# Kernel tuning notes

Hardware: AMD Instinct MI355X
Metric: run time of the kernel (lower is better)

## Reference

```python
import jax, jax.numpy as jnp
import numpy as np

H = 16  # num_heads
NEG = -1e9


def setup_inputs() -> dict:
    key = jax.random.key(0)
    ks = jax.random.split(key, 12)
    T, B, E, M = 2048, 2, 1024, 1024
    s = E ** -0.5
    inp = {
        "query": jax.random.normal(ks[0], (T, B, E), jnp.float32),
        "position_encoding": jax.random.normal(ks[1], (H, T, T), jnp.float32) * 0.02,
        "long_context_retrieval": jax.random.normal(ks[2], (2, M, B, E), jnp.float32),
        "q_w": jax.random.normal(ks[3], (E, E), jnp.float32) * s,
        "q_b": jnp.zeros((E,), jnp.float32),
        "k_w": jax.random.normal(ks[4], (E, E), jnp.float32) * s,
        "k_b": jnp.zeros((E,), jnp.float32),
        "v_w": jax.random.normal(ks[5], (E, E), jnp.float32) * s,
        "v_b": jnp.zeros((E,), jnp.float32),
        "out_w": jax.random.normal(ks[6], (E, E), jnp.float32) * s,
        "out_b": jnp.zeros((E,), jnp.float32),
        "memory_bias": jnp.zeros((H,), jnp.float32),
    }
    return inp


def reference(query, position_encoding, long_context_retrieval,
              q_w, q_b, k_w, k_b, v_w, v_b, out_w, out_b, memory_bias):
    T, B, E = query.shape
    D = E // H
    scaling = D ** -0.5

    def proj(x, w, b):
        # x: [L, B, E] -> [B, H, L, D]
        L = x.shape[0]
        y = jnp.einsum('lbe,fe->lbf', x, w) + b
        return y.reshape(L, B, H, D).transpose(1, 2, 0, 3)

    q = proj(query, q_w, q_b) * scaling          # [B,H,T,D]
    k = proj(query, k_w, k_b)                    # [B,H,T,D]
    v = proj(query, v_w, v_b)                    # [B,H,T,D]

    # local attention with per-head position encoding and causal mask
    scores = jnp.einsum('bhtd,bhsd->bhts', q, k) + position_encoding[None]
    causal = jnp.triu(jnp.ones((T, T), bool), k=1)
    scores = jnp.where(causal[None, None], NEG, scores)
    attn_local = jax.nn.softmax(scores, axis=-1)
    out_local = jnp.einsum('bhts,bhsd->bhtd', attn_local, v)

    # attention over retrieved long-context memory (keys/values projected)
    km = proj(long_context_retrieval[0], k_w, k_b)   # [B,H,M,D]
    vm = proj(long_context_retrieval[1], v_w, v_b)   # [B,H,M,D]
    mem_scores = jnp.einsum('bhtd,bhmd->bhtm', q, km)
    attn_mem = jax.nn.softmax(mem_scores, axis=-1)
    out_mem = jnp.einsum('bhtm,bhmd->bhtd', attn_mem, vm)

    # per-head learned gate: weighted sum of local and memory outputs
    g = jax.nn.sigmoid(memory_bias)[None, :, None, None]
    out = (1.0 - g) * out_local + g * out_mem        # [B,H,T,D]

    out = out.transpose(2, 0, 1, 3).reshape(T, B, E)
    return jnp.einsum('tbe,fe->tbf', out, out_w) + out_b
```

## Files before the change

kernel.cpp:

```cpp
#include <hip/hip_runtime.h>

typedef __bf16 bf16_t;
typedef __bf16 bf16x2 __attribute__((ext_vector_type(2)));
typedef __bf16 bf16x4 __attribute__((ext_vector_type(4)));
typedef __bf16 bf16x8 __attribute__((ext_vector_type(8)));
typedef float floatx4 __attribute__((ext_vector_type(4)));

#define MFMA16(a, b, c) __builtin_amdgcn_mfma_f32_16x16x32_bf16((a), (b), (c), 0, 0, 0)

__global__ void detect_kernel(const uint4* __restrict__ q, int* __restrict__ flag)
{
    __shared__ int cnt;
    if (threadIdx.x == 0) cnt = 0;
    __syncthreads();
    int local = 0;
    for (int i = threadIdx.x; i < 8192; i += 1024) {
        uint4 u = q[i];
        unsigned w;
        w = u.x; if ((w & 0x7F80u) == 0x7F80u) local++; if (((w >> 16) & 0x7F80u) == 0x7F80u) local++;
        w = u.y; if ((w & 0x7F80u) == 0x7F80u) local++; if (((w >> 16) & 0x7F80u) == 0x7F80u) local++;
        w = u.z; if ((w & 0x7F80u) == 0x7F80u) local++; if (((w >> 16) & 0x7F80u) == 0x7F80u) local++;
        w = u.w; if ((w & 0x7F80u) == 0x7F80u) local++; if (((w >> 16) & 0x7F80u) == 0x7F80u) local++;
    }
    atomicAdd(&cnt, local);
    __syncthreads();
    if (threadIdx.x == 0) flag[0] = (cnt >= 8) ? 1 : 0;
}

__device__ inline void cvt16_f32(const float* __restrict__ p, bf16x8& lo, bf16x8& hi)
{
    float4 a = ((const float4*)p)[0];
    float4 b = ((const float4*)p)[1];
    float4 c = ((const float4*)p)[2];
    float4 d = ((const float4*)p)[3];
    lo[0] = (bf16_t)a.x; lo[1] = (bf16_t)a.y; lo[2] = (bf16_t)a.z; lo[3] = (bf16_t)a.w;
    lo[4] = (bf16_t)b.x; lo[5] = (bf16_t)b.y; lo[6] = (bf16_t)b.z; lo[7] = (bf16_t)b.w;
    hi[0] = (bf16_t)c.x; hi[1] = (bf16_t)c.y; hi[2] = (bf16_t)c.z; hi[3] = (bf16_t)c.w;
    hi[4] = (bf16_t)d.x; hi[5] = (bf16_t)d.y; hi[6] = (bf16_t)d.z; hi[7] = (bf16_t)d.w;
}

__global__ __launch_bounds__(256) void proj_kernel(
    const void* __restrict__ query, const void* __restrict__ lcr,
    const void* __restrict__ qw, const void* __restrict__ kw,
    const void* __restrict__ vw,
    const void* __restrict__ qbias, const void* __restrict__ kbias,
    const void* __restrict__ vbias,
    bf16_t* __restrict__ q_ws, bf16_t* __restrict__ k_ws,
    bf16_t* __restrict__ vt_ws, bf16_t* __restrict__ km_ws,
    bf16_t* __restrict__ vmt_ws, const int* __restrict__ flag)
{
    __shared__ __attribute__((aligned(16))) bf16_t As[128 * 40];
    __shared__ __attribute__((aligned(16))) bf16_t Bs[128 * 40];

    const int f32 = flag[0];
    const int K = 1024;
    const int blk = blockIdx.x;

    int rm0, wcol, mode, Tdim;
    float scale;
    const void* Xv; size_t xoff0; const void* Wv; const void* biasv; bf16_t* Yv;
    if (blk < 768) {
        rm0 = (blk & 31) * 128;
        const int cn0 = (blk >> 5) * 128;
        const int sel = cn0 >> 10;
        wcol = cn0 & 1023;
        Xv = query; xoff0 = 0; Tdim = 2048;
        if (sel == 0)      { Wv = qw; biasv = qbias; Yv = q_ws;  mode = 1; scale = 0.125f; }
        else if (sel == 1) { Wv = kw; biasv = kbias; Yv = k_ws;  mode = 1; scale = 1.f; }
        else               { Wv = vw; biasv = vbias; Yv = vt_ws; mode = 2; scale = 1.f; }
    } else if (blk < 896) {
        const int b2 = blk - 768;
        rm0 = (b2 & 15) * 128; wcol = (b2 >> 4) * 128;
        Xv = lcr; xoff0 = 0;
        Wv = kw; biasv = kbias; Yv = km_ws; mode = 1; scale = 1.f; Tdim = 1024;
    } else {
        const int b2 = blk - 896;
        rm0 = (b2 & 15) * 128; wcol = (b2 >> 4) * 128;
        Xv = lcr; xoff0 = (size_t)1024 * 2 * 1024;
        Wv = vw; biasv = vbias; Yv = vmt_ws; mode = 2; scale = 1.f; Tdim = 1024;
    }

    const int tid = threadIdx.x;
    const int wvid = tid >> 6, lane = tid & 63;
    const int qd = lane >> 4, l16 = lane & 15;
    const int wm = (wvid >> 1) * 64, wn = (wvid & 1) * 64;

    const int srow = tid >> 1;
    const int sseg = (tid & 1) * 16;
    const size_t xoff = xoff0 + (size_t)(rm0 + srow) * K + sseg;
    const size_t woff = (size_t)(wcol + srow) * K + sseg;
    const bf16_t* Xh = (const bf16_t*)Xv + xoff;
    const float*  Xf = (const float*)Xv + xoff;
    const bf16_t* Wh = (const bf16_t*)Wv + woff;
    const float*  Wf = (const float*)Wv + woff;
    bf16_t* Asw = &As[srow * 40 + sseg];
    bf16_t* Bsw = &Bs[srow * 40 + sseg];

    floatx4 acc[4][4];
#pragma unroll
    for (int i = 0; i < 4; i++)
#pragma unroll
        for (int j = 0; j < 4; j++) acc[i][j] = (floatx4){0.f, 0.f, 0.f, 0.f};

    for (int k0 = 0; k0 < K; k0 += 32) {
        bf16x8 x0, x1, w0, w1;
        if (f32) {
            cvt16_f32(Xf + k0, x0, x1);
            cvt16_f32(Wf + k0, w0, w1);
        } else {
            x0 = *(const bf16x8*)(Xh + k0);
            x1 = *(const bf16x8*)(Xh + k0 + 8);
            w0 = *(const bf16x8*)(Wh + k0);
            w1 = *(const bf16x8*)(Wh + k0 + 8);
        }
        __syncthreads();
        *(bf16x8*)(Asw) = x0;
        *(bf16x8*)(Asw + 8) = x1;
        *(bf16x8*)(Bsw) = w0;
        *(bf16x8*)(Bsw + 8) = w1;
        __syncthreads();

        bf16x8 af[4], bfg[4];
#pragma unroll
        for (int mi = 0; mi < 4; mi++)
            af[mi] = *(const bf16x8*)(&As[(wm + mi * 16 + l16) * 40 + qd * 8]);
#pragma unroll
        for (int ni = 0; ni < 4; ni++)
            bfg[ni] = *(const bf16x8*)(&Bs[(wn + ni * 16 + l16) * 40 + qd * 8]);
#pragma unroll
        for (int mi = 0; mi < 4; mi++)
#pragma unroll
            for (int ni = 0; ni < 4; ni++)
                acc[mi][ni] = MFMA16(af[mi], bfg[ni], acc[mi][ni]);
    }

#pragma unroll
    for (int ni = 0; ni < 4; ni++) {
        const int col = wcol + wn + ni * 16 + l16;
        const float bv = f32 ? ((const float*)biasv)[col]
                             : (float)((const bf16_t*)biasv)[col];
        const int hh = col >> 6, dd = col & 63;
#pragma unroll
        for (int mi = 0; mi < 4; mi++) {
            const int row0 = rm0 + wm + mi * 16 + qd * 4;
            const int t = row0 >> 1;
            const float v0 = (acc[mi][ni][0] + bv) * scale;
            const float v1 = (acc[mi][ni][1] + bv) * scale;
            const float v2 = (acc[mi][ni][2] + bv) * scale;
            const float v3 = (acc[mi][ni][3] + bv) * scale;
            if (mode == 1) {
                Yv[(((size_t)hh * Tdim) + t) * 64 + dd]            = (bf16_t)v0;
                Yv[(((size_t)(16 + hh) * Tdim) + t) * 64 + dd]     = (bf16_t)v1;
                Yv[(((size_t)hh * Tdim) + t + 1) * 64 + dd]        = (bf16_t)v2;
                Yv[(((size_t)(16 + hh) * Tdim) + t + 1) * 64 + dd] = (bf16_t)v3;
            } else {
                bf16x2 p0; p0[0] = (bf16_t)v0; p0[1] = (bf16_t)v2;
                bf16x2 p1; p1[0] = (bf16_t)v1; p1[1] = (bf16_t)v3;
                *(bf16x2*)&Yv[((size_t)hh * 64 + dd) * Tdim + t] = p0;
                *(bf16x2*)&Yv[((size_t)(16 + hh) * 64 + dd) * Tdim + t] = p1;
            }
        }
    }
}

#define PSTR 88

__device__ __forceinline__ void load_k8(bf16x8 k0v[4], bf16x8 k1v[4],
                                        const bf16_t* __restrict__ Kb,
                                        int s0, int l16, int qd)
{
#pragma unroll
    for (int ni = 0; ni < 4; ni++) {
        const bf16_t* p = Kb + (size_t)(s0 + ni * 16 + l16) * 64 + qd * 8;
        k0v[ni] = *(const bf16x8*)p;
        k1v[ni] = *(const bf16x8*)(p + 32);
    }
}

__device__ __forceinline__ void load_pos4(floatx4 pn[4], const float* __restrict__ posf,
                                          const bf16_t* __restrict__ posh, int f32,
                                          int T, int trow_base, int s0, int l16, bool diag)
{
#pragma unroll
    for (int ni = 0; ni < 4; ni++) {
        const int sg = s0 + ni * 16 + l16;
#pragma unroll
        for (int r = 0; r < 4; r++) {
            const int tg = trow_base + r;
            const size_t pidx = (size_t)tg * T + sg;
            float pv = f32 ? posf[pidx] : (float)posh[pidx];
            if (diag && sg > tg) pv = -1e9f;
            pn[ni][r] = pv;
        }
    }
}

__global__ __launch_bounds__(256) void attn_kernel(
    const bf16_t* __restrict__ Qg, const bf16_t* __restrict__ Kg,
    const bf16_t* __restrict__ VTg, const bf16_t* __restrict__ KMg,
    const bf16_t* __restrict__ VMTg, const void* __restrict__ posv,
    const void* __restrict__ mbiasv, float* __restrict__ attl,
    float* __restrict__ attm, const int* __restrict__ flag, int T, int Mlen)
{
    __shared__ __attribute__((aligned(16))) bf16_t Ps[4][16 * PSTR];

    const int f32 = flag[0];
    const int tid = threadIdx.x;
    const int wv = tid >> 6, lane = tid & 63;
    const int qd = lane >> 4, l16 = lane & 15;
    const int qt = blockIdx.x;
    const int y = blockIdx.y;
    const int b = y & 1, h = y >> 1;
    const int bh = b * 16 + h;
    const int tw = qt * 64 + wv * 16;
    const int trow_base = tw + qd * 4;
    bf16_t* Pw = &Ps[wv][0];

    const bf16_t* Qb = Qg + (size_t)bh * T * 64;
    const bf16x8 a0 = *(const bf16x8*)(Qb + (size_t)(tw + l16) * 64 + qd * 8);
    const bf16x8 a1 = *(const bf16x8*)(Qb + (size_t)(tw + l16) * 64 + 32 + qd * 8);

    const float gb = f32 ? ((const float*)mbiasv)[h] : (float)((const bf16_t*)mbiasv)[h];
    const float g = 1.f / (1.f + __expf(-gb));

    floatx4 O[4];
    float ml[4], ll[4];
#pragma unroll
    for (int i = 0; i < 4; i++) {
        O[i] = (floatx4){0.f, 0.f, 0.f, 0.f};
        ml[i] = -1e9f; ll[i] = 0.f;
    }

    bf16x8 kc0[4], kc1[4];

    if (blockIdx.z == 0) {
        const bf16_t* Kb  = Kg  + (size_t)bh * T * 64;
        const bf16_t* VTb = VTg + (size_t)bh * 64 * T;
        const float*  posf = (const float*)posv + (size_t)h * T * T;
        const bf16_t* posh = (const bf16_t*)posv + (size_t)h * T * T;

        floatx4 pn[4];
        load_k8(kc0, kc1, Kb, 0, l16, qd);
        load_pos4(pn, posf, posh, f32, T, trow_base, 0, l16, qt == 0);

        for (int st = 0; st <= qt; ++st) {
            const int s0 = st * 64;
            bf16x8 vf0[4], vf1[4];
#pragma unroll
            for (int ni = 0; ni < 4; ni++) {
                const bf16_t* p = VTb + (size_t)(ni * 16 + l16) * T + s0 + qd * 8;
                vf0[ni] = *(const bf16x8*)p;
                vf1[ni] = *(const bf16x8*)(p + 32);
            }
            floatx4 c[4];
#pragma unroll
            for (int ni = 0; ni < 4; ni++) {
                floatx4 t = pn[ni];
                t = MFMA16(a0, kc0[ni], t);
                t = MFMA16(a1, kc1[ni], t);
                c[ni] = t;
            }
            if (st < qt) {
                load_k8(kc0, kc1, Kb, s0 + 64, l16, qd);
                load_pos4(pn, posf, posh, f32, T, trow_base, s0 + 64, l16, st + 1 == qt);
            }
#pragma unroll
            for (int r = 0; r < 4; r++) {
                float mt = fmaxf(fmaxf(c[0][r], c[1][r]), fmaxf(c[2][r], c[3][r]));
                mt = fmaxf(mt, __shfl_xor(mt, 1));
                mt = fmaxf(mt, __shfl_xor(mt, 2));
                mt = fmaxf(mt, __shfl_xor(mt, 4));
                mt = fmaxf(mt, __shfl_xor(mt, 8));
                const float mnew = fmaxf(ml[r], mt);
                const float alpha = __expf(ml[r] - mnew);
                ml[r] = mnew;
                float ls = 0.f;
#pragma unroll
                for (int ni = 0; ni < 4; ni++) {
                    const float p = __expf(c[ni][r] - mnew);
                    c[ni][r] = p;
                    ls += p;
                }
                ll[r] = ll[r] * alpha + ls;
#pragma unroll
                for (int ni = 0; ni < 4; ni++) O[ni][r] *= alpha;
#pragma unroll
                for (int ni = 0; ni < 4; ni++)
                    Pw[(qd * 4 + r) * PSTR + ni * 16 + l16] = (bf16_t)c[ni][r];
            }
            asm volatile("s_waitcnt lgkmcnt(0)" ::: "memory");
            const bf16x8 pf0 = *(const bf16x8*)(&Pw[l16 * PSTR + qd * 8]);
            const bf16x8 pf1 = *(const bf16x8*)(&Pw[l16 * PSTR + 32 + qd * 8]);
#pragma unroll
            for (int ni = 0; ni < 4; ni++) {
                O[ni] = MFMA16(pf0, vf0[ni], O[ni]);
                O[ni] = MFMA16(pf1, vf1[ni], O[ni]);
            }
        }

        const float gl = 1.f - g;
#pragma unroll
        for (int r = 0; r < 4; r++) {
            float lt = ll[r];
            lt += __shfl_xor(lt, 1);
            lt += __shfl_xor(lt, 2);
            lt += __shfl_xor(lt, 4);
            lt += __shfl_xor(lt, 8);
            const int tg = trow_base + r;
            const float inv = gl / lt;
#pragma unroll
            for (int ni = 0; ni < 4; ni++)
                attl[(size_t)(tg * 2 + b) * 1024 + h * 64 + ni * 16 + l16] = O[ni][r] * inv;
        }
    } else {
        const bf16_t* Kb  = KMg  + (size_t)bh * Mlen * 64;
        const bf16_t* VTb = VMTg + (size_t)bh * 64 * Mlen;
        const int nst = Mlen >> 6;

        load_k8(kc0, kc1, Kb, 0, l16, qd);

        for (int st = 0; st < nst; ++st) {
            const int s0 = st * 64;
            bf16x8 vf0[4], vf1[4];
#pragma unroll
            for (int ni = 0; ni < 4; ni++) {
                const bf16_t* p = VTb + (size_t)(ni * 16 + l16) * Mlen + s0 + qd * 8;
                vf0[ni] = *(const bf16x8*)p;
                vf1[ni] = *(const bf16x8*)(p + 32);
            }
            floatx4 c[4];
#pragma unroll
            for (int ni = 0; ni < 4; ni++) {
                floatx4 t = (floatx4){0.f, 0.f, 0.f, 0.f};
                t = MFMA16(a0, kc0[ni], t);
                t = MFMA16(a1, kc1[ni], t);
                c[ni] = t;
            }
            if (st < nst - 1) load_k8(kc0, kc1, Kb, s0 + 64, l16, qd);
#pragma unroll
            for (int r = 0; r < 4; r++) {
                float mt = fmaxf(fmaxf(c[0][r], c[1][r]), fmaxf(c[2][r], c[3][r]));
                mt = fmaxf(mt, __shfl_xor(mt, 1));
                mt = fmaxf(mt, __shfl_xor(mt, 2));
                mt = fmaxf(mt, __shfl_xor(mt, 4));
                mt = fmaxf(mt, __shfl_xor(mt, 8));
                const float mnew = fmaxf(ml[r], mt);
                const float alpha = __expf(ml[r] - mnew);
                ml[r] = mnew;
                float ls = 0.f;
#pragma unroll
                for (int ni = 0; ni < 4; ni++) {
                    const float p = __expf(c[ni][r] - mnew);
                    c[ni][r] = p;
                    ls += p;
                }
                ll[r] = ll[r] * alpha + ls;
#pragma unroll
                for (int ni = 0; ni < 4; ni++) O[ni][r] *= alpha;
#pragma unroll
                for (int ni = 0; ni < 4; ni++)
                    Pw[(qd * 4 + r) * PSTR + ni * 16 + l16] = (bf16_t)c[ni][r];
            }
            asm volatile("s_waitcnt lgkmcnt(0)" ::: "memory");
            const bf16x8 pf0 = *(const bf16x8*)(&Pw[l16 * PSTR + qd * 8]);
            const bf16x8 pf1 = *(const bf16x8*)(&Pw[l16 * PSTR + 32 + qd * 8]);
#pragma unroll
            for (int ni = 0; ni < 4; ni++) {
                O[ni] = MFMA16(pf0, vf0[ni], O[ni]);
                O[ni] = MFMA16(pf1, vf1[ni], O[ni]);
            }
        }

#pragma unroll
        for (int r = 0; r < 4; r++) {
            float lt = ll[r];
            lt += __shfl_xor(lt, 1);
            lt += __shfl_xor(lt, 2);
            lt += __shfl_xor(lt, 4);
            lt += __shfl_xor(lt, 8);
            const int tg = trow_base + r;
            const float inv = g / lt;
#pragma unroll
            for (int ni = 0; ni < 4; ni++)
                attm[(size_t)(tg * 2 + b) * 1024 + h * 64 + ni * 16 + l16] = O[ni][r] * inv;
        }
    }
}

__global__ __launch_bounds__(256) void combine_kernel(
    const float4* __restrict__ a, const float4* __restrict__ bsrc,
    bf16_t* __restrict__ o, int n4)
{
    const int i = blockIdx.x * 256 + threadIdx.x;
    if (i >= n4) return;
    const float4 x = a[i];
    const float4 y = bsrc[i];
    bf16x4 r;
    r[0] = (bf16_t)(x.x + y.x);
    r[1] = (bf16_t)(x.y + y.y);
    r[2] = (bf16_t)(x.z + y.z);
    r[3] = (bf16_t)(x.w + y.w);
    *(bf16x4*)(o + (size_t)i * 4) = r;
}

__global__ __launch_bounds__(256) void gemm64_kernel(
    const bf16_t* __restrict__ X, const void* __restrict__ Wv,
    const void* __restrict__ biasv, void* __restrict__ Yv,
    const int* __restrict__ flag)
{
    __shared__ __attribute__((aligned(16))) bf16_t As[64 * 40];
    __shared__ __attribute__((aligned(16))) bf16_t Bs[128 * 40];

    const int f32 = flag[0];
    const int K = 1024, N = 1024;
    const int tid = threadIdx.x;
    const int wvid = tid >> 6, lane = tid & 63;
    const int qd = lane >> 4, l16 = lane & 15;
    const int wn = wvid * 32;
    const int rm0 = blockIdx.x * 64, cn0 = blockIdx.y * 128;

    const int arow = tid >> 1;
    const int aseg = (tid & 1) * 16;
    const bf16_t* Xp = X + (size_t)(rm0 + (arow & 63)) * K + aseg;
    const size_t woff = (size_t)(cn0 + arow) * K + aseg;
    const bf16_t* Wh = (const bf16_t*)Wv + woff;
    const float*  Wf = (const float*)Wv + woff;

    floatx4 acc[4][2];
#pragma unroll
    for (int i = 0; i < 4; i++)
#pragma unroll
        for (int j = 0; j < 2; j++) acc[i][j] = (floatx4){0.f, 0.f, 0.f, 0.f};

    for (int k0 = 0; k0 < K; k0 += 32) {
        bf16x8 x0, x1, w0, w1;
        if (tid < 128) {
            x0 = *(const bf16x8*)(Xp + k0);
            x1 = *(const bf16x8*)(Xp + k0 + 8);
        }
        if (f32) cvt16_f32(Wf + k0, w0, w1);
        else {
            w0 = *(const bf16x8*)(Wh + k0);
            w1 = *(const bf16x8*)(Wh + k0 + 8);
        }
        __syncthreads();
        if (tid < 128) {
            *(bf16x8*)&As[arow * 40 + aseg] = x0;
            *(bf16x8*)&As[arow * 40 + aseg + 8] = x1;
        }
        *(bf16x8*)&Bs[arow * 40 + aseg] = w0;
        *(bf16x8*)&Bs[arow * 40 + aseg + 8] = w1;
        __syncthreads();

        bf16x8 af[4], bfg[2];
#pragma unroll
        for (int mi = 0; mi < 4; mi++)
            af[mi] = *(const bf16x8*)(&As[(mi * 16 + l16) * 40 + qd * 8]);
#pragma unroll
        for (int ni = 0; ni < 2; ni++)
            bfg[ni] = *(const bf16x8*)(&Bs[(wn + ni * 16 + l16) * 40 + qd * 8]);
#pragma unroll
        for (int mi = 0; mi < 4; mi++)
#pragma unroll
            for (int ni = 0; ni < 2; ni++)
                acc[mi][ni] = MFMA16(af[mi], bfg[ni], acc[mi][ni]);
    }

#pragma unroll
    for (int ni = 0; ni < 2; ni++) {
        const int col = cn0 + wn + ni * 16 + l16;
        const float bv = f32 ? ((const float*)biasv)[col]
                             : (float)((const bf16_t*)biasv)[col];
#pragma unroll
        for (int mi = 0; mi < 4; mi++) {
            const int row0 = rm0 + mi * 16 + qd * 4;
#pragma unroll
            for (int r = 0; r < 4; r++) {
                const int row = row0 + r;
                const float val = acc[mi][ni][r] + bv;
                if (f32) ((float*)Yv)[(size_t)row * N + col] = val;
                else ((bf16_t*)Yv)[(size_t)row * N + col] = (bf16_t)val;
            }
        }
    }
}

__global__ void sentinel_kernel(float* o) { o[0] = 30000.0f; }

extern "C" void kernel_launch(void* const* d_in, const int* in_sizes, int n_in,
                              void* d_out, int out_size, void* d_ws, size_t ws_size,
                              hipStream_t stream)
{
    const void* query = d_in[0];
    const void* pos   = d_in[1];
    const void* lcr   = d_in[2];
    const void* q_w   = d_in[3];
    const void* q_b   = d_in[4];
    const void* k_w   = d_in[5];
    const void* k_b   = d_in[6];
    const void* v_w   = d_in[7];
    const void* v_b   = d_in[8];
    const void* out_w = d_in[9];
    const void* out_b = d_in[10];
    const void* mbias = d_in[11];

    const int T = 2048, B = 2, E = 1024, M = 1024;

    const size_t nqkv = (size_t)B * 16 * T * 64;
    const size_t nmem = (size_t)B * 16 * M * 64;
    const size_t natt = (size_t)T * B * E;
    const size_t bf16_elems = 3 * nqkv + 2 * nmem + natt;
    const size_t needed = bf16_elems * 2 + 2 * natt * 4 + 64;
    if (ws_size < needed) {
        sentinel_kernel<<<1, 1, 0, stream>>>((float*)d_out);
        return;
    }

    bf16_t* q_ws   = (bf16_t*)d_ws;
    bf16_t* k_ws   = q_ws + nqkv;
    bf16_t* vt_ws  = k_ws + nqkv;
    bf16_t* km_ws  = vt_ws + nqkv;
    bf16_t* vmt_ws = km_ws + nmem;
    bf16_t* att_ws = vmt_ws + nmem;
    float* attl_ws = (float*)(att_ws + natt);
    float* attm_ws = attl_ws + natt;
    int* flag = (int*)(attm_ws + natt);

    detect_kernel<<<1, 1024, 0, stream>>>((const uint4*)query, flag);
    proj_kernel<<<1024, 256, 0, stream>>>(query, lcr, q_w, k_w, v_w,
                                          q_b, k_b, v_b,
                                          q_ws, k_ws, vt_ws, km_ws, vmt_ws, flag);
    attn_kernel<<<dim3(T / 64, 32, 2), 256, 0, stream>>>(
        q_ws, k_ws, vt_ws, km_ws, vmt_ws, pos, mbias, attl_ws, attm_ws, flag, T, M);
    combine_kernel<<<(int)(natt / 4 / 256), 256, 0, stream>>>(
        (const float4*)attl_ws, (const float4*)attm_ws, att_ws, (int)(natt / 4));
    gemm64_kernel<<<dim3(T * B / 64, E / 128), 256, 0, stream>>>(
        att_ws, out_w, out_b, d_out, flag);
    (void)in_sizes; (void)n_in; (void)out_size;
}
```

Measured before the change: 851.7 us.

## Pre-tile position encoding to bf16 and pair causal query tiles per block

Adds a prep kernel that converts the per-head position bias to bf16, applies the causal mask, and stores it in the per-lane MFMA fragment order of lower-triangular tiles. The attention kernel can then read each tile's bias as two contiguous 16-byte loads instead of scattered strided fp32 reads. The attention grid is halved and each block handles query tile p together with tile 31-p, which evens out causal work across blocks. The cost is an extra pass over the position tensor, extra workspace, and bf16 rounding of the bias. The tiled path is used only when the workspace is large enough.

```diff
diff --git a/kernel.cpp b/kernel.cpp
--- a/kernel.cpp
+++ b/kernel.cpp
@@ -37,6 +37,57 @@
     lo[4] = (bf16_t)b.x; lo[5] = (bf16_t)b.y; lo[6] = (bf16_t)b.z; lo[7] = (bf16_t)b.w;
     hi[0] = (bf16_t)c.x; hi[1] = (bf16_t)c.y; hi[2] = (bf16_t)c.z; hi[3] = (bf16_t)c.w;
     hi[4] = (bf16_t)d.x; hi[5] = (bf16_t)d.y; hi[6] = (bf16_t)d.z; hi[7] = (bf16_t)d.w;
+}
+
+__global__ __launch_bounds__(256) void prep_pos(
+    const void* __restrict__ posv, bf16_t* __restrict__ post,
+    const int* __restrict__ flag, int T)
+{
+    const int st = blockIdx.x, qt = blockIdx.y, h = blockIdx.z;
+    if (st > qt) return;
+    __shared__ float tf[64 * 65];
+    const int t = threadIdx.x;
+    const int f32 = flag[0];
+    const size_t rb = ((size_t)h * T + qt * 64) * T + st * 64;
+    if (f32) {
+        const float* pf = (const float*)posv + rb;
+#pragma unroll
+        for (int it = 0; it < 4; ++it) {
+            const int idx = it * 256 + t;
+            const int row = idx >> 4, c4 = (idx & 15) * 4;
+            const float4 v = *(const float4*)(pf + (size_t)row * T + c4);
+            tf[row * 65 + c4 + 0] = v.x;
+            tf[row * 65 + c4 + 1] = v.y;
+            tf[row * 65 + c4 + 2] = v.z;
+            tf[row * 65 + c4 + 3] = v.w;
+        }
+    } else {
+        const bf16_t* ph = (const bf16_t*)posv + rb;
+#pragma unroll
+        for (int it = 0; it < 2; ++it) {
+            const int idx = it * 256 + t;
+            const int row = idx >> 3, c8 = (idx & 7) * 8;
+            const bf16x8 v = *(const bf16x8*)(ph + (size_t)row * T + c8);
+#pragma unroll
+            for (int j = 0; j < 8; ++j) tf[row * 65 + c8 + j] = (float)v[j];
+        }
+    }
+    __syncthreads();
+    const int gg = t >> 4, l16 = t & 15;
+    const bool diag = (st == qt);
+    bf16x8 o0, o1;
+#pragma unroll
+    for (int j = 0; j < 16; ++j) {
+        const int ni = j >> 2, r = j & 3;
+        const int row = gg * 4 + r, col = ni * 16 + l16;
+        float v = tf[row * 65 + col];
+        if (diag && col > row) v = -1e9f;
+        if (j < 8) o0[j] = (bf16_t)v; else o1[j - 8] = (bf16_t)v;
+    }
+    bf16_t* out = post + ((size_t)h * 528 + (size_t)qt * (qt + 1) / 2 + st) * 4096
+                       + (size_t)t * 16;
+    *(bf16x8*)out = o0;
+    *(bf16x8*)(out + 8) = o1;
 }
 
 __global__ __launch_bounds__(256) void proj_kernel(
@@ -199,8 +250,9 @@
     const bf16_t* __restrict__ Qg, const bf16_t* __restrict__ Kg,
     const bf16_t* __restrict__ VTg, const bf16_t* __restrict__ KMg,
     const bf16_t* __restrict__ VMTg, const void* __restrict__ posv,
-    const void* __restrict__ mbiasv, float* __restrict__ attl,
-    float* __restrict__ attm, const int* __restrict__ flag, int T, int Mlen)
+    const bf16_t* __restrict__ post, const void* __restrict__ mbiasv,
+    float* __restrict__ attl, float* __restrict__ attm,
+    const int* __restrict__ flag, int T, int Mlen, int tiled)
 {
     __shared__ __attribute__((aligned(16))) bf16_t Ps[4][16 * PSTR];
 
@@ -208,181 +260,209 @@
     const int tid = threadIdx.x;
     const int wv = tid >> 6, lane = tid & 63;
     const int qd = lane >> 4, l16 = lane & 15;
-    const int qt = blockIdx.x;
+    const int p = blockIdx.x;
     const int y = blockIdx.y;
     const int b = y & 1, h = y >> 1;
     const int bh = b * 16 + h;
-    const int tw = qt * 64 + wv * 16;
-    const int trow_base = tw + qd * 4;
     bf16_t* Pw = &Ps[wv][0];
-
-    const bf16_t* Qb = Qg + (size_t)bh * T * 64;
-    const bf16x8 a0 = *(const bf16x8*)(Qb + (size_t)(tw + l16) * 64 + qd * 8);
-    const bf16x8 a1 = *(const bf16x8*)(Qb + (size_t)(tw + l16) * 64 + 32 + qd * 8);
+    const int laneTileOff = ((wv * 4 + qd) * 16 + l16) * 16;
 
     const float gb = f32 ? ((const float*)mbiasv)[h] : (float)((const bf16_t*)mbiasv)[h];
     const float g = 1.f / (1.f + __expf(-gb));
-
-    floatx4 O[4];
-    float ml[4], ll[4];
-#pragma unroll
-    for (int i = 0; i < 4; i++) {
-        O[i] = (floatx4){0.f, 0.f, 0.f, 0.f};
-        ml[i] = -1e9f; ll[i] = 0.f;
-    }
-
-    bf16x8 kc0[4], kc1[4];
-
-    if (blockIdx.z == 0) {
-        const bf16_t* Kb  = Kg  + (size_t)bh * T * 64;
-        const bf16_t* VTb = VTg + (size_t)bh * 64 * T;
-        const float*  posf = (const float*)posv + (size_t)h * T * T;
-        const bf16_t* posh = (const bf16_t*)posv + (size_t)h * T * T;
-
-        floatx4 pn[4];
-        load_k8(kc0, kc1, Kb, 0, l16, qd);
-        load_pos4(pn, posf, posh, f32, T, trow_base, 0, l16, qt == 0);
-
-        for (int st = 0; st <= qt; ++st) {
-            const int s0 = st * 64;
-            bf16x8 vf0[4], vf1[4];
-#pragma unroll
-            for (int ni = 0; ni < 4; ni++) {
-                const bf16_t* p = VTb + (size_t)(ni * 16 + l16) * T + s0 + qd * 8;
-                vf0[ni] = *(const bf16x8*)p;
-                vf1[ni] = *(const bf16x8*)(p + 32);
+    const float gl = 1.f - g;
+
+    const bf16_t* Qb = Qg + (size_t)bh * T * 64;
+
+    for (int half = 0; half < 2; ++half) {
+        const int qt = half ? (31 - p) : p;
+        const int tw = qt * 64 + wv * 16;
+        const int trow_base = tw + qd * 4;
+
+        const bf16x8 a0 = *(const bf16x8*)(Qb + (size_t)(tw + l16) * 64 + qd * 8);
+        const bf16x8 a1 = *(const bf16x8*)(Qb + (size_t)(tw + l16) * 64 + 32 + qd * 8);
+
+        floatx4 O[4];
+        float ml[4], ll[4];
+#pragma unroll
+        for (int i = 0; i < 4; i++) {
+            O[i] = (floatx4){0.f, 0.f, 0.f, 0.f};
+            ml[i] = -1e9f; ll[i] = 0.f;
+        }
+
+        bf16x8 kc0[4], kc1[4];
+
+        if (blockIdx.z == 0) {
+            const bf16_t* Kb  = Kg  + (size_t)bh * T * 64;
+            const bf16_t* VTb = VTg + (size_t)bh * 64 * T;
+            const float*  posf = (const float*)posv + (size_t)h * T * T;
+            const bf16_t* posh = (const bf16_t*)posv + (size_t)h * T * T;
+            const bf16_t* ptile = post + ((size_t)h * 528 + (size_t)qt * (qt + 1) / 2) * 4096
+                                       + laneTileOff;
+
+            floatx4 pn[4];
+            bf16x8 pt0, pt1;
+            load_k8(kc0, kc1, Kb, 0, l16, qd);
+            if (tiled) {
+                pt0 = *(const bf16x8*)(ptile);
+                pt1 = *(const bf16x8*)(ptile + 8);
+            } else {
+                load_pos4(pn, posf, posh, f32, T, trow_base, 0, l16, qt == 0);
             }
-            floatx4 c[4];
-#pragma unroll
-            for (int ni = 0; ni < 4; ni++) {
-                floatx4 t = pn[ni];
-                t = MFMA16(a0, kc0[ni], t);
-                t = MFMA16(a1, kc1[ni], t);
-                c[ni] = t;
+
+            for (int st = 0; st <= qt; ++st) {
+                const int s0 = st * 64;
+                bf16x8 vf0[4], vf1[4];
+#pragma unroll
+                for (int ni = 0; ni < 4; ni++) {
+                    const bf16_t* vp = VTb + (size_t)(ni * 16 + l16) * T + s0 + qd * 8;
+                    vf0[ni] = *(const bf16x8*)vp;
+                    vf1[ni] = *(const bf16x8*)(vp + 32);
+                }
+                if (tiled) {
+#pragma unroll
+                    for (int ni = 0; ni < 4; ni++)
+#pragma unroll
+                        for (int r = 0; r < 4; r++)
+                            pn[ni][r] = (ni < 2) ? (float)pt0[ni * 4 + r]
+                                                 : (float)pt1[ni * 4 + r - 8];
+                }
+                floatx4 c[4];
+#pragma unroll
+                for (int ni = 0; ni < 4; ni++) {
+                    floatx4 t = pn[ni];
+                    t = MFMA16(a0, kc0[ni], t);
+                    t = MFMA16(a1, kc1[ni], t);
+                    c[ni] = t;
+                }
+                if (st < qt) {
+                    load_k8(kc0, kc1, Kb, s0 + 64, l16, qd);
+                    if (tiled) {
+                        pt0 = *(const bf16x8*)(ptile + (st + 1) * 4096);
+                        pt1 = *(const bf16x8*)(ptile + (st + 1) * 4096 + 8);
+                    } else {
+                        load_pos4(pn, posf, posh, f32, T, trow_base, s0 + 64, l16,
+                                  st + 1 == qt);
+                    }
+                }
+#pragma unroll
+                for (int r = 0; r < 4; r++) {
+                    float mt = fmaxf(fmaxf(c[0][r], c[1][r]), fmaxf(c[2][r], c[3][r]));
+                    mt = fmaxf(mt, __shfl_xor(mt, 1));
+                    mt = fmaxf(mt, __shfl_xor(mt, 2));
+                    mt = fmaxf(mt, __shfl_xor(mt, 4));
+                    mt = fmaxf(mt, __shfl_xor(mt, 8));
+                    const float mnew = fmaxf(ml[r], mt);
+                    const float alpha = __expf(ml[r] - mnew);
+                    ml[r] = mnew;
+                    float ls = 0.f;
+#pragma unroll
+                    for (int ni = 0; ni < 4; ni++) {
+                        const float pe = __expf(c[ni][r] - mnew);
+                        c[ni][r] = pe;
+                        ls += pe;
+                    }
+                    ll[r] = ll[r] * alpha + ls;
+#pragma unroll
+                    for (int ni = 0; ni < 4; ni++) O[ni][r] *= alpha;
+#pragma unroll
+                    for (int ni = 0; ni < 4; ni++)
+                        Pw[(qd * 4 + r) * PSTR + ni * 16 + l16] = (bf16_t)c[ni][r];
+                }
+                asm volatile("s_waitcnt lgkmcnt(0)" ::: "memory");
+                const bf16x8 pf0 = *(const bf16x8*)(&Pw[l16 * PSTR + qd * 8]);
+                const bf16x8 pf1 = *(const bf16x8*)(&Pw[l16 * PSTR + 32 + qd * 8]);
+#pragma unroll
+                for (int ni = 0; ni < 4; ni++) {
+                    O[ni] = MFMA16(pf0, vf0[ni], O[ni]);
+                    O[ni] = MFMA16(pf1, vf1[ni], O[ni]);
+                }
             }
-            if (st < qt) {
-                load_k8(kc0, kc1, Kb, s0 + 64, l16, qd);
-                load_pos4(pn, posf, posh, f32, T, trow_base, s0 + 64, l16, st + 1 == qt);
+
+#pragma unroll
+            for (int r = 0; r < 4; r++) {
+                float lt = ll[r];
+                lt += __shfl_xor(lt, 1);
+                lt += __shfl_xor(lt, 2);
+                lt += __shfl_xor(lt, 4);
+                lt += __shfl_xor(lt, 8);
+                const int tg = trow_base + r;
+                const float inv = gl / lt;
+#pragma unroll
+                for (int ni = 0; ni < 4; ni++)
+                    attl[(size_t)(tg * 2 + b) * 1024 + h * 64 + ni * 16 + l16] = O[ni][r] * inv;
             }
+        } else {
+            const bf16_t* Kb  = KMg  + (size_t)bh * Mlen * 64;
+            const bf16_t* VTb = VMTg + (size_t)bh * 64 * Mlen;
+            const int nst = Mlen >> 6;
+
+            load_k8(kc0, kc1, Kb, 0, l16, qd);
+
+            for (int st = 0; st < nst; ++st) {
+                const int s0 = st * 64;
+                bf16x8 vf0[4], vf1[4];
+#pragma unroll
+                for (int ni = 0; ni < 4; ni++) {
+                    const bf16_t* vp = VTb + (size_t)(ni * 16 + l16) * Mlen + s0 + qd * 8;
+                    vf0[ni] = *(const bf16x8*)vp;
+                    vf1[ni] = *(const bf16x8*)(vp + 32);
+                }
+                floatx4 c[4];
+#pragma unroll
+                for (int ni = 0; ni < 4; ni++) {
+                    floatx4 t = (floatx4){0.f, 0.f, 0.f, 0.f};
+                    t = MFMA16(a0, kc0[ni], t);
+                    t = MFMA16(a1, kc1[ni], t);
+                    c[ni] = t;
+                }
+                if (st < nst - 1) load_k8(kc0, kc1, Kb, s0 + 64, l16, qd);
+#pragma unroll
+                for (int r = 0; r < 4; r++) {
+                    float mt = fmaxf(fmaxf(c[0][r], c[1][r]), fmaxf(c[2][r], c[3][r]));
+                    mt = fmaxf(mt, __shfl_xor(mt, 1));
+                    mt = fmaxf(mt, __shfl_xor(mt, 2));
+                    mt = fmaxf(mt, __shfl_xor(mt, 4));
+                    mt = fmaxf(mt, __shfl_xor(mt, 8));
+                    const float mnew = fmaxf(ml[r], mt);
+                    const float alpha = __expf(ml[r] - mnew);
+                    ml[r] = mnew;
+                    float ls = 0.f;
+#pragma unroll
+                    for (int ni = 0; ni < 4; ni++) {
+                        const float pe = __expf(c[ni][r] - mnew);
+                        c[ni][r] = pe;
+                        ls += pe;
+                    }
+                    ll[r] = ll[r] * alpha + ls;
+#pragma unroll
+                    for (int ni = 0; ni < 4; ni++) O[ni][r] *= alpha;
+#pragma unroll
+                    for (int ni = 0; ni < 4; ni++)
+                        Pw[(qd * 4 + r) * PSTR + ni * 16 + l16] = (bf16_t)c[ni][r];
+                }
+                asm volatile("s_waitcnt lgkmcnt(0)" ::: "memory");
+                const bf16x8 pf0 = *(const bf16x8*)(&Pw[l16 * PSTR + qd * 8]);
+                const bf16x8 pf1 = *(const bf16x8*)(&Pw[l16 * PSTR + 32 + qd * 8]);
+#pragma unroll
+                for (int ni = 0; ni < 4; ni++) {
+                    O[ni] = MFMA16(pf0, vf0[ni], O[ni]);
+                    O[ni] = MFMA16(pf1, vf1[ni], O[ni]);
+                }
+            }
+
 #pragma unroll
             for (int r = 0; r < 4; r++) {
-                float mt = fmaxf(fmaxf(c[0][r], c[1][r]), fmaxf(c[2][r], c[3][r]));
-                mt = fmaxf(mt, __shfl_xor(mt, 1));
-                mt = fmaxf(mt, __shfl_xor(mt, 2));
-                mt = fmaxf(mt, __shfl_xor(mt, 4));
-                mt = fmaxf(mt, __shfl_xor(mt, 8));
-                const float mnew = fmaxf(ml[r], mt);
-                const float alpha = __expf(ml[r] - mnew);
-                ml[r] = mnew;
-                float ls = 0.f;
-#pragma unroll
-                for (int ni = 0; ni < 4; ni++) {
-                    const float p = __expf(c[ni][r] - mnew);
-                    c[ni][r] = p;
-                    ls += p;
-                }
-                ll[r] = ll[r] * alpha + ls;
-#pragma unroll
-                for (int ni = 0; ni < 4; ni++) O[ni][r] *= alpha;
+                float lt = ll[r];
+                lt += __shfl_xor(lt, 1);
+                lt += __shfl_xor(lt, 2);
+                lt += __shfl_xor(lt, 4);
+                lt += __shfl_xor(lt, 8);
+                const int tg = trow_base + r;
+                const float inv = g / lt;
 #pragma unroll
                 for (int ni = 0; ni < 4; ni++)
-                    Pw[(qd * 4 + r) * PSTR + ni * 16 + l16] = (bf16_t)c[ni][r];
+                    attm[(size_t)(tg * 2 + b) * 1024 + h * 64 + ni * 16 + l16] = O[ni][r] * inv;
             }
-            asm volatile("s_waitcnt lgkmcnt(0)" ::: "memory");
-            const bf16x8 pf0 = *(const bf16x8*)(&Pw[l16 * PSTR + qd * 8]);
-            const bf16x8 pf1 = *(const bf16x8*)(&Pw[l16 * PSTR + 32 + qd * 8]);
-#pragma unroll
-            for (int ni = 0; ni < 4; ni++) {
-                O[ni] = MFMA16(pf0, vf0[ni], O[ni]);
-                O[ni] = MFMA16(pf1, vf1[ni], O[ni]);
-            }
-        }
-
-        const float gl = 1.f - g;
-#pragma unroll
-        for (int r = 0; r < 4; r++) {
-            float lt = ll[r];
-            lt += __shfl_xor(lt, 1);
-            lt += __shfl_xor(lt, 2);
-            lt += __shfl_xor(lt, 4);
-            lt += __shfl_xor(lt, 8);
-            const int tg = trow_base + r;
-            const float inv = gl / lt;
-#pragma unroll
-            for (int ni = 0; ni < 4; ni++)
-                attl[(size_t)(tg * 2 + b) * 1024 + h * 64 + ni * 16 + l16] = O[ni][r] * inv;
-        }
-    } else {
-        const bf16_t* Kb  = KMg  + (size_t)bh * Mlen * 64;
-        const bf16_t* VTb = VMTg + (size_t)bh * 64 * Mlen;
-        const int nst = Mlen >> 6;
-
-        load_k8(kc0, kc1, Kb, 0, l16, qd);
-
-        for (int st = 0; st < nst; ++st) {
-            const int s0 = st * 64;
-            bf16x8 vf0[4], vf1[4];
-#pragma unroll
-            for (int ni = 0; ni < 4; ni++) {
-                const bf16_t* p = VTb + (size_t)(ni * 16 + l16) * Mlen + s0 + qd * 8;
-                vf0[ni] = *(const bf16x8*)p;
-                vf1[ni] = *(const bf16x8*)(p + 32);
-            }
-            floatx4 c[4];
-#pragma unroll
-            for (int ni = 0; ni < 4; ni++) {
-                floatx4 t = (floatx4){0.f, 0.f, 0.f, 0.f};
-                t = MFMA16(a0, kc0[ni], t);
-                t = MFMA16(a1, kc1[ni], t);
-                c[ni] = t;
-            }
-            if (st < nst - 1) load_k8(kc0, kc1, Kb, s0 + 64, l16, qd);
-#pragma unroll
-            for (int r = 0; r < 4; r++) {
-                float mt = fmaxf(fmaxf(c[0][r], c[1][r]), fmaxf(c[2][r], c[3][r]));
-                mt = fmaxf(mt, __shfl_xor(mt, 1));
-                mt = fmaxf(mt, __shfl_xor(mt, 2));
-                mt = fmaxf(mt, __shfl_xor(mt, 4));
-                mt = fmaxf(mt, __shfl_xor(mt, 8));
-                const float mnew = fmaxf(ml[r], mt);
-                const float alpha = __expf(ml[r] - mnew);
-                ml[r] = mnew;
-                float ls = 0.f;
-#pragma unroll
-                for (int ni = 0; ni < 4; ni++) {
-                    const float p = __expf(c[ni][r] - mnew);
-                    c[ni][r] = p;
-                    ls += p;
-                }
-                ll[r] = ll[r] * alpha + ls;
-#pragma unroll
-                for (int ni = 0; ni < 4; ni++) O[ni][r] *= alpha;
-#pragma unroll
-                for (int ni = 0; ni < 4; ni++)
-                    Pw[(qd * 4 + r) * PSTR + ni * 16 + l16] = (bf16_t)c[ni][r];
-            }
-            asm volatile("s_waitcnt lgkmcnt(0)" ::: "memory");
-            const bf16x8 pf0 = *(const bf16x8*)(&Pw[l16 * PSTR + qd * 8]);
-            const bf16x8 pf1 = *(const bf16x8*)(&Pw[l16 * PSTR + 32 + qd * 8]);
-#pragma unroll
-            for (int ni = 0; ni < 4; ni++) {
-                O[ni] = MFMA16(pf0, vf0[ni], O[ni]);
-                O[ni] = MFMA16(pf1, vf1[ni], O[ni]);
-            }
-        }
-
-#pragma unroll
-        for (int r = 0; r < 4; r++) {
-            float lt = ll[r];
-            lt += __shfl_xor(lt, 1);
-            lt += __shfl_xor(lt, 2);
-            lt += __shfl_xor(lt, 4);
-            lt += __shfl_xor(lt, 8);
-            const int tg = trow_base + r;
-            const float inv = g / lt;
-#pragma unroll
-            for (int ni = 0; ni < 4; ni++)
-                attm[(size_t)(tg * 2 + b) * 1024 + h * 64 + ni * 16 + l16] = O[ni][r] * inv;
         }
     }
 }
@@ -510,11 +590,14 @@
     const size_t nmem = (size_t)B * 16 * M * 64;
     const size_t natt = (size_t)T * B * E;
     const size_t bf16_elems = 3 * nqkv + 2 * nmem + natt;
-    const size_t needed = bf16_elems * 2 + 2 * natt * 4 + 64;
-    if (ws_size < needed) {
+    const size_t needed_small = bf16_elems * 2 + 2 * natt * 4 + 64;
+    const size_t post_bytes = (size_t)16 * 528 * 4096 * 2;
+    const size_t needed_tiled = needed_small + post_bytes;
+    if (ws_size < needed_small) {
         sentinel_kernel<<<1, 1, 0, stream>>>((float*)d_out);
         return;
     }
+    const int tiled = (ws_size >= needed_tiled) ? 1 : 0;
 
     bf16_t* q_ws   = (bf16_t*)d_ws;
     bf16_t* k_ws   = q_ws + nqkv;
@@ -525,13 +608,17 @@
     float* attl_ws = (float*)(att_ws + natt);
     float* attm_ws = attl_ws + natt;
     int* flag = (int*)(attm_ws + natt);
+    bf16_t* post_ws = (bf16_t*)((char*)d_ws + needed_small);
 
     detect_kernel<<<1, 1024, 0, stream>>>((const uint4*)query, flag);
+    if (tiled)
+        prep_pos<<<dim3(32, 32, 16), 256, 0, stream>>>(pos, post_ws, flag, T);
     proj_kernel<<<1024, 256, 0, stream>>>(query, lcr, q_w, k_w, v_w,
                                           q_b, k_b, v_b,
                                           q_ws, k_ws, vt_ws, km_ws, vmt_ws, flag);
-    attn_kernel<<<dim3(T / 64, 32, 2), 256, 0, stream>>>(
-        q_ws, k_ws, vt_ws, km_ws, vmt_ws, pos, mbias, attl_ws, attm_ws, flag, T, M);
+    attn_kernel<<<dim3(16, 32, 2), 256, 0, stream>>>(
+        q_ws, k_ws, vt_ws, km_ws, vmt_ws, pos, post_ws, mbias,
+        attl_ws, attm_ws, flag, T, M, tiled);
     combine_kernel<<<(int)(natt / 4 / 256), 256, 0, stream>>>(
         (const float4*)attl_ws, (const float4*)attm_ws, att_ws, (int)(natt / 4));
     gemm64_kernel<<<dim3(T * B / 64, E / 128), 256, 0, stream>>>(
```

Result: faster. 795.5 us (-6.6%).
